# Optimization experiments

Hardware: AMD Instinct MI355X
Metric: run time of the kernel (lower is better)

Reference implementation:

```python
import jax, jax.numpy as jnp
import numpy as np

B, T, D_IN, D_OUT = 4, 2048, 4096, 16384
MAX_INT = 127   # 2**(8-1) - 1
MIN_INT = -128  # -2**(8-1)
THRESH = 0.5
EPS = 1e-8


def setup_inputs() -> dict:
    key = jax.random.key(0)
    kx, kw, kb = jax.random.split(key, 3)
    x = jax.random.normal(kx, (B, T, D_IN), dtype=jnp.float32)
    # kaiming_uniform_(a=sqrt(5)) -> uniform(-1/sqrt(fan_in), 1/sqrt(fan_in))
    bound = 1.0 / np.sqrt(D_IN)
    weight = jax.random.uniform(kw, (D_OUT, D_IN), minval=-bound, maxval=bound, dtype=jnp.float32)
    bias = jax.random.uniform(kb, (D_OUT,), minval=-bound, maxval=bound, dtype=jnp.float32)
    return {"x": x, "weight": weight, "bias": bias}


def reference(x, weight, bias):
    # Per-token 8-bit absmax activation quantization (simulated)
    scale = jnp.max(jnp.abs(x), axis=-1, keepdims=True) / MAX_INT  # (B,T,1)
    x_int = jnp.clip(jnp.round(x / (scale + EPS)), MIN_INT, MAX_INT)
    x_q = x_int * scale
    # Ternary absmean weight quantization with STE
    w_scale = jnp.mean(jnp.abs(weight))
    w_scaled = weight / (w_scale + EPS)
    W_q = jnp.sign(w_scaled) * (jnp.abs(w_scaled) > THRESH).astype(weight.dtype)
    W_ste = weight + jax.lax.stop_gradient(W_q - weight)
    # Dense GEMM on dequantized values: (B,T,D_in) x (D_out,D_in)^T
    return jnp.einsum('btd,od->bto', x_q, W_ste) + bias
```

## Files before the change

kernel.cpp:

```cpp
#include <hip/hip_runtime.h>
#include <stdint.h>

#define B_DIM 4
#define T_DIM 2048
#define D_IN  4096
#define D_OUT 16384
#define M_DIM (B_DIM * T_DIM)
#define NW    ((size_t)D_OUT * (size_t)D_IN)

typedef __attribute__((ext_vector_type(4))) int v4i;

__global__ __launch_bounds__(256) void act_quant_kernel(
    const float* __restrict__ x, int8_t* __restrict__ xq,
    float* __restrict__ scales) {
  const int row = blockIdx.x;
  const float4* xr = (const float4*)(x + (size_t)row * D_IN);
  float4 v[4];
  float amax = 0.f;
#pragma unroll
  for (int c = 0; c < 4; ++c) {
    v[c] = xr[c * 256 + threadIdx.x];
    amax = fmaxf(amax, fmaxf(fmaxf(fabsf(v[c].x), fabsf(v[c].y)),
                             fmaxf(fabsf(v[c].z), fabsf(v[c].w))));
  }
#pragma unroll
  for (int off = 32; off > 0; off >>= 1)
    amax = fmaxf(amax, __shfl_down(amax, off, 64));
  __shared__ float smax[4];
  const int lane = threadIdx.x & 63, wave = threadIdx.x >> 6;
  if (lane == 0) smax[wave] = amax;
  __syncthreads();
  amax = fmaxf(fmaxf(smax[0], smax[1]), fmaxf(smax[2], smax[3]));
  const float scale = amax * (1.0f / 127.0f);
  const float denom = scale + 1e-8f;
  if (threadIdx.x == 0) scales[row] = scale;
  int* outp = (int*)(xq + (size_t)row * D_IN);
#pragma unroll
  for (int c = 0; c < 4; ++c) {
    int q0 = min(127, max(-128, __float2int_rn(v[c].x / denom)));
    int q1 = min(127, max(-128, __float2int_rn(v[c].y / denom)));
    int q2 = min(127, max(-128, __float2int_rn(v[c].z / denom)));
    int q3 = min(127, max(-128, __float2int_rn(v[c].w / denom)));
    outp[c * 256 + threadIdx.x] =
        (q0 & 255) | ((q1 & 255) << 8) | ((q2 & 255) << 16) | ((q3 & 255) << 24);
  }
}

__global__ __launch_bounds__(256) void wabs_kernel(const float* __restrict__ w,
                                                   double* __restrict__ out) {
  const float4* w4 = (const float4*)w;
  const size_t n4 = NW / 4;
  double acc = 0.0;
  for (size_t i = (size_t)blockIdx.x * blockDim.x + threadIdx.x; i < n4;
       i += (size_t)gridDim.x * blockDim.x) {
    float4 v = w4[i];
    acc += (double)fabsf(v.x) + (double)fabsf(v.y);
    acc += (double)fabsf(v.z) + (double)fabsf(v.w);
  }
#pragma unroll
  for (int off = 32; off > 0; off >>= 1) acc += __shfl_down(acc, off, 64);
  __shared__ double ssum[4];
  const int lane = threadIdx.x & 63, wave = threadIdx.x >> 6;
  if (lane == 0) ssum[wave] = acc;
  __syncthreads();
  if (threadIdx.x == 0) atomicAdd(out, ssum[0] + ssum[1] + ssum[2] + ssum[3]);
}

__global__ __launch_bounds__(256) void wquant_kernel(
    const float* __restrict__ w, const double* __restrict__ sumAbs,
    int8_t* __restrict__ wq) {
  const float ws = (float)(*sumAbs / (double)NW) + 1e-8f;
  const float4* w4 = (const float4*)w;
  int* outp = (int*)wq;
  const size_t stride = (size_t)gridDim.x * blockDim.x;
  size_t i = (size_t)blockIdx.x * blockDim.x + threadIdx.x;
#pragma unroll
  for (int c = 0; c < 4; ++c, i += stride) {
    float4 v = w4[i];
    float t0 = v.x / ws, t1 = v.y / ws, t2 = v.z / ws, t3 = v.w / ws;
    int q0 = (fabsf(t0) > 0.5f) ? ((t0 > 0.f) ? 1 : -1) : 0;
    int q1 = (fabsf(t1) > 0.5f) ? ((t1 > 0.f) ? 1 : -1) : 0;
    int q2 = (fabsf(t2) > 0.5f) ? ((t2 > 0.f) ? 1 : -1) : 0;
    int q3 = (fabsf(t3) > 0.5f) ? ((t3 > 0.f) ? 1 : -1) : 0;
    outp[i] = (q0 & 255) | ((q1 & 255) << 8) | ((q2 & 255) << 16) | ((q3 & 255) << 24);
  }
}

#define BM 256
#define BN 256
#define BKB 128
#define NKT (D_IN / BKB)
#define A0s 0
#define B0s 32768
#define A1s 65536
#define B1s 98304

#define BARRIER() __builtin_amdgcn_s_barrier()
#define VMWAIT(n) asm volatile("s_waitcnt vmcnt(" #n ")" ::: "memory")
#define LGKM0()   asm volatile("s_waitcnt lgkmcnt(0)" ::: "memory")

__global__ __launch_bounds__(512, 2) void gemm_i8_kernel(
    const int8_t* __restrict__ xq, const int8_t* __restrict__ wq,
    const float* __restrict__ scales, const float* __restrict__ bias,
    float* __restrict__ out) {
  __shared__ __align__(16) int8_t lds[131072];

  const int tid = threadIdx.x;
  const int lane = tid & 63;
  const int wave = tid >> 6;
  const int wr = wave >> 2;
  const int wc = wave & 3;
  const int quad = lane >> 4;
  const int r16 = lane & 15;

  const int bid = blockIdx.x;
  const int swz = (bid & 7) * 256 + (bid >> 3);
  const int bm = (swz >> 6) * BM;
  const int bn = (swz & 63) * BN;

  const int sr = tid >> 3;
  const int scol = ((tid & 7) << 4) ^ ((sr & 7) << 4);
  const int8_t* gA = xq + (size_t)(bm + sr) * D_IN + scol;
  const int8_t* gB = wq + (size_t)(bn + sr) * D_IN + scol;

#define STAGE(opbase, gp, q, kt)                                          \
  __builtin_amdgcn_global_load_lds(                                       \
      (const __attribute__((address_space(1))) void*)((gp) +              \
          (size_t)(q) * (64 * D_IN) + (kt) * BKB),                        \
      (__attribute__((address_space(3))) void*)(lds + (opbase) +          \
          (q) * 8192 + tid * 16),                                         \
      16, 0, 0);

  const int sw = (r16 & 7) << 4;
  int koff[2];
  koff[0] = (quad * 16) ^ sw;
  koff[1] = (quad * 16 + 64) ^ sw;
  const int arow = wr * 128 + r16;
  const int brow = wc * 64 + r16;

  v4i acc[8][4] = {};
  v4i a[4][2], b[4][2];

#define LDA(base, h)                                                      \
  _Pragma("unroll") for (int i = 0; i < 4; ++i) {                         \
    _Pragma("unroll") for (int kk = 0; kk < 2; ++kk)                      \
        a[i][kk] = *(const v4i*)&lds[(base) +                             \
            (arow + (h) * 64 + i * 16) * BKB + koff[kk]];                 \
  }
#define LDB(base, j0)                                                     \
  _Pragma("unroll") for (int j = 0; j < 2; ++j) {                         \
    _Pragma("unroll") for (int kk = 0; kk < 2; ++kk)                      \
        b[(j0) + j][kk] = *(const v4i*)&lds[(base) +                      \
            (brow + ((j0) + j) * 16) * BKB + koff[kk]];                   \
  }
#define MM(h, j0)                                                         \
  LGKM0();                                                                \
  __builtin_amdgcn_s_setprio(1);                                          \
  _Pragma("unroll") for (int kk = 0; kk < 2; ++kk) {                      \
    _Pragma("unroll") for (int i = 0; i < 4; ++i) {                       \
      _Pragma("unroll") for (int j = 0; j < 2; ++j)                       \
          acc[(h) * 4 + i][(j0) + j] =                                    \
              __builtin_amdgcn_mfma_i32_16x16x64_i8(                      \
                  a[i][kk], b[(j0) + j][kk],                              \
                  acc[(h) * 4 + i][(j0) + j], 0, 0, 0);                   \
    }                                                                     \
  }                                                                       \
  __builtin_amdgcn_s_setprio(0);

  STAGE(A0s, gA, 0, 0) STAGE(A0s, gA, 1, 0) STAGE(A0s, gA, 2, 0) STAGE(A0s, gA, 3, 0)
  STAGE(B0s, gB, 0, 0) STAGE(B0s, gB, 1, 0) STAGE(B0s, gB, 2, 0) STAGE(B0s, gB, 3, 0)
  STAGE(A1s, gA, 0, 1) STAGE(A1s, gA, 2, 1)
  STAGE(B1s, gB, 0, 1) STAGE(B1s, gB, 1, 1) STAGE(B1s, gB, 2, 1) STAGE(B1s, gB, 3, 1)
  VMWAIT(6);
  BARRIER();

#pragma unroll 1
  for (int t = 0; t < NKT / 2; ++t) {
    const int kt1 = 2 * t + 1;
    const int kt2 = (2 * t + 2) & (NKT - 1);
    const int kt3 = (2 * t + 3) & (NKT - 1);
    LDA(A0s, 0) LDB(B0s, 0)
    STAGE(A1s, gA, 1, kt1) STAGE(A1s, gA, 3, kt1)
    BARRIER();
    MM(0, 0)
    BARRIER();
    LDB(B0s, 2)
    STAGE(A0s, gA, 0, kt2) STAGE(A0s, gA, 2, kt2)
    BARRIER();
    MM(0, 2)
    BARRIER();
    LDA(A0s, 1)
    STAGE(B0s, gB, 0, kt2) STAGE(B0s, gB, 1, kt2)
    BARRIER();
    MM(1, 2)
    BARRIER();
    STAGE(B0s, gB, 2, kt2) STAGE(B0s, gB, 3, kt2)
    BARRIER();
    MM(1, 0)
    VMWAIT(6);
    BARRIER();
    LDA(A1s, 0) LDB(B1s, 0)
    STAGE(A0s, gA, 1, kt2) STAGE(A0s, gA, 3, kt2)
    BARRIER();
    MM(0, 0)
    BARRIER();
    LDB(B1s, 2)
    STAGE(A1s, gA, 0, kt3) STAGE(A1s, gA, 2, kt3)
    BARRIER();
    MM(0, 2)
    BARRIER();
    LDA(A1s, 1)
    STAGE(B1s, gB, 0, kt3) STAGE(B1s, gB, 1, kt3)
    BARRIER();
    MM(1, 2)
    BARRIER();
    STAGE(B1s, gB, 2, kt3) STAGE(B1s, gB, 3, kt3)
    BARRIER();
    MM(1, 0)
    VMWAIT(6);
    BARRIER();
  }
  VMWAIT(0);

  float bs[4];
#pragma unroll
  for (int j = 0; j < 4; ++j) bs[j] = bias[bn + wc * 64 + j * 16 + r16];

#pragma unroll
  for (int i = 0; i < 8; ++i) {
#pragma unroll
    for (int reg = 0; reg < 4; ++reg) {
      const int m = bm + wr * 128 + i * 16 + quad * 4 + reg;
      const float s = scales[m];
      float* orow = out + (size_t)m * D_OUT + bn + wc * 64 + r16;
#pragma unroll
      for (int j = 0; j < 4; ++j) {
        orow[j * 16] = (float)acc[i][j][reg] * s + bs[j];
      }
    }
  }
}

extern "C" void kernel_launch(void* const* d_in, const int* in_sizes, int n_in,
                              void* d_out, int out_size, void* d_ws,
                              size_t ws_size, hipStream_t stream) {
  const float* x = (const float*)d_in[0];
  const float* w = (const float*)d_in[1];
  const float* bias = (const float*)d_in[2];
  float* out = (float*)d_out;

  char* ws = (char*)d_ws;
  double* d_sum = (double*)ws;
  float* d_scales = (float*)(ws + 256);
  int8_t* d_xq = (int8_t*)(ws + 33024);
  int8_t* d_wq = (int8_t*)(ws + 33024 + (size_t)M_DIM * D_IN);

  hipMemsetAsync(d_sum, 0, sizeof(double), stream);

  act_quant_kernel<<<M_DIM, 256, 0, stream>>>(x, d_xq, d_scales);
  wabs_kernel<<<2048, 256, 0, stream>>>(w, d_sum);
  wquant_kernel<<<16384, 256, 0, stream>>>(w, d_sum, d_wq);
  gemm_i8_kernel<<<2048, 512, 0, stream>>>(d_xq, d_wq, d_scales, bias, out);
}
```

Measured before the change: 1.250 ms.

## Prefetch LDS fragments earlier in GEMM and make weight-sum reduction deterministic

```diff
diff --git a/kernel.cpp b/kernel.cpp
--- a/kernel.cpp
+++ b/kernel.cpp
@@ -47,7 +47,7 @@
 }
 
 __global__ __launch_bounds__(256) void wabs_kernel(const float* __restrict__ w,
-                                                   double* __restrict__ out) {
+                                                   double* __restrict__ partial) {
   const float4* w4 = (const float4*)w;
   const size_t n4 = NW / 4;
   double acc = 0.0;
@@ -63,7 +63,21 @@
   const int lane = threadIdx.x & 63, wave = threadIdx.x >> 6;
   if (lane == 0) ssum[wave] = acc;
   __syncthreads();
-  if (threadIdx.x == 0) atomicAdd(out, ssum[0] + ssum[1] + ssum[2] + ssum[3]);
+  if (threadIdx.x == 0)
+    partial[blockIdx.x] = ssum[0] + ssum[1] + ssum[2] + ssum[3];
+}
+
+__global__ __launch_bounds__(256) void wsum_kernel(
+    const double* __restrict__ partial, double* __restrict__ out) {
+  double acc = 0.0;
+  for (int i = threadIdx.x; i < 2048; i += 256) acc += partial[i];
+#pragma unroll
+  for (int off = 32; off > 0; off >>= 1) acc += __shfl_down(acc, off, 64);
+  __shared__ double ssum[4];
+  const int lane = threadIdx.x & 63, wave = threadIdx.x >> 6;
+  if (lane == 0) ssum[wave] = acc;
+  __syncthreads();
+  if (threadIdx.x == 0) out[0] = ssum[0] + ssum[1] + ssum[2] + ssum[3];
 }
 
 __global__ __launch_bounds__(256) void wquant_kernel(
@@ -97,7 +111,6 @@
 
 #define BARRIER() __builtin_amdgcn_s_barrier()
 #define VMWAIT(n) asm volatile("s_waitcnt vmcnt(" #n ")" ::: "memory")
-#define LGKM0()   asm volatile("s_waitcnt lgkmcnt(0)" ::: "memory")
 
 __global__ __launch_bounds__(512, 2) void gemm_i8_kernel(
     const int8_t* __restrict__ xq, const int8_t* __restrict__ wq,
@@ -141,20 +154,16 @@
   v4i acc[8][4] = {};
   v4i a[4][2], b[4][2];
 
-#define LDA(base, h)                                                      \
-  _Pragma("unroll") for (int i = 0; i < 4; ++i) {                         \
-    _Pragma("unroll") for (int kk = 0; kk < 2; ++kk)                      \
-        a[i][kk] = *(const v4i*)&lds[(base) +                             \
-            (arow + (h) * 64 + i * 16) * BKB + koff[kk]];                 \
-  }
-#define LDB(base, j0)                                                     \
-  _Pragma("unroll") for (int j = 0; j < 2; ++j) {                         \
-    _Pragma("unroll") for (int kk = 0; kk < 2; ++kk)                      \
-        b[(j0) + j][kk] = *(const v4i*)&lds[(base) +                      \
-            (brow + ((j0) + j) * 16) * BKB + koff[kk]];                   \
-  }
+#define LDQA(base, h, kk)                                                 \
+  _Pragma("unroll") for (int i = 0; i < 4; ++i)                           \
+      a[i][kk] = *(const v4i*)&lds[(base) +                               \
+          (arow + (h) * 64 + i * 16) * BKB + koff[kk]];
+#define LDQB(base, j0, kk)                                                \
+  _Pragma("unroll") for (int j = 0; j < 2; ++j)                           \
+      b[(j0) + j][kk] = *(const v4i*)&lds[(base) +                        \
+          (brow + ((j0) + j) * 16) * BKB + koff[kk]];
+
 #define MM(h, j0)                                                         \
-  LGKM0();                                                                \
   __builtin_amdgcn_s_setprio(1);                                          \
   _Pragma("unroll") for (int kk = 0; kk < 2; ++kk) {                      \
     _Pragma("unroll") for (int i = 0; i < 4; ++i) {                       \
@@ -179,17 +188,17 @@
     const int kt1 = 2 * t + 1;
     const int kt2 = (2 * t + 2) & (NKT - 1);
     const int kt3 = (2 * t + 3) & (NKT - 1);
-    LDA(A0s, 0) LDB(B0s, 0)
+    LDQA(A0s, 0, 0) LDQB(B0s, 0, 0) LDQA(A0s, 0, 1) LDQB(B0s, 0, 1)
+    LDQB(B0s, 2, 0) LDQB(B0s, 2, 1)
     STAGE(A1s, gA, 1, kt1) STAGE(A1s, gA, 3, kt1)
     BARRIER();
     MM(0, 0)
     BARRIER();
-    LDB(B0s, 2)
     STAGE(A0s, gA, 0, kt2) STAGE(A0s, gA, 2, kt2)
     BARRIER();
     MM(0, 2)
     BARRIER();
-    LDA(A0s, 1)
+    LDQA(A0s, 1, 0) LDQA(A0s, 1, 1)
     STAGE(B0s, gB, 0, kt2) STAGE(B0s, gB, 1, kt2)
     BARRIER();
     MM(1, 2)
@@ -199,17 +208,17 @@
     MM(1, 0)
     VMWAIT(6);
     BARRIER();
-    LDA(A1s, 0) LDB(B1s, 0)
+    LDQA(A1s, 0, 0) LDQB(B1s, 0, 0) LDQA(A1s, 0, 1) LDQB(B1s, 0, 1)
+    LDQB(B1s, 2, 0) LDQB(B1s, 2, 1)
     STAGE(A0s, gA, 1, kt2) STAGE(A0s, gA, 3, kt2)
     BARRIER();
     MM(0, 0)
     BARRIER();
-    LDB(B1s, 2)
     STAGE(A1s, gA, 0, kt3) STAGE(A1s, gA, 2, kt3)
     BARRIER();
     MM(0, 2)
     BARRIER();
-    LDA(A1s, 1)
+    LDQA(A1s, 1, 0) LDQA(A1s, 1, 1)
     STAGE(B1s, gB, 0, kt3) STAGE(B1s, gB, 1, kt3)
     BARRIER();
     MM(1, 2)
@@ -251,14 +260,14 @@
 
   char* ws = (char*)d_ws;
   double* d_sum = (double*)ws;
-  float* d_scales = (float*)(ws + 256);
-  int8_t* d_xq = (int8_t*)(ws + 33024);
-  int8_t* d_wq = (int8_t*)(ws + 33024 + (size_t)M_DIM * D_IN);
-
-  hipMemsetAsync(d_sum, 0, sizeof(double), stream);
+  double* d_partial = (double*)(ws + 256);
+  float* d_scales = (float*)(ws + 16640);
+  int8_t* d_xq = (int8_t*)(ws + 49408);
+  int8_t* d_wq = (int8_t*)(ws + 49408 + (size_t)M_DIM * D_IN);
 
   act_quant_kernel<<<M_DIM, 256, 0, stream>>>(x, d_xq, d_scales);
-  wabs_kernel<<<2048, 256, 0, stream>>>(w, d_sum);
+  wabs_kernel<<<2048, 256, 0, stream>>>(w, d_partial);
+  wsum_kernel<<<1, 256, 0, stream>>>(d_partial, d_sum);
   wquant_kernel<<<16384, 256, 0, stream>>>(w, d_sum, d_wq);
   gemm_i8_kernel<<<2048, 512, 0, stream>>>(d_xq, d_wq, d_scales, bias, out);
 }
```

Result: no change. 1.249 ms (-0.1%).
